# Performance work log

Measured on AMD Instinct MI355X. Metric: run time of the kernel, lower is better.

## Reference

```python
import jax, jax.numpy as jnp
import numpy as np

H = 768
L = 4096
P, KP = 8192, 8
EV, KE = 2048, 6
E = 16384
NR = 32
NUM_LABELS = 2


def setup_inputs() -> dict:
    key = jax.random.key(0)
    ks = jax.random.split(key, 10)
    seq = jax.random.normal(ks[0], (1, L, H), dtype=jnp.float32)
    phrase_idx = jax.random.randint(ks[1], (P, KP), 0, L, dtype=jnp.int32)
    phrase_mask = jnp.ones((P, KP), dtype=jnp.float32)
    event_idx = jax.random.randint(ks[2], (EV, KE), 0, L, dtype=jnp.int32)
    event_mask = jnp.ones((EV, KE), dtype=jnp.float32)
    pair_idx = jax.random.randint(ks[3], (E, 2), 0, EV, dtype=jnp.int32)
    root_idx = jax.random.randint(ks[4], (NR,), 0, P, dtype=jnp.int32)
    s1 = 1.0 / np.sqrt(2 * H)
    W1 = jax.random.normal(ks[5], (2 * H, H), dtype=jnp.float32) * s1
    b1 = jnp.zeros((H,), dtype=jnp.float32)
    Wb = jax.random.normal(ks[6], (2 * H, NUM_LABELS), dtype=jnp.float32) * s1
    bb = jnp.zeros((NUM_LABELS,), dtype=jnp.float32)
    return {"seq": seq, "phrase_idx": phrase_idx, "phrase_mask": phrase_mask,
            "event_idx": event_idx, "event_mask": event_mask, "pair_idx": pair_idx,
            "root_idx": root_idx, "W1": W1, "b1": b1, "Wb": Wb, "bb": bb}


def _masked_mean_gather(tok, idx, mask):
    # tok: [L,H]; idx: [N,K] int; mask: [N,K] float -> [N,H]
    g = tok[idx]                                  # [N,K,H] irregular gather
    s = jnp.einsum('nkh,nk->nh', g, mask)
    d = jnp.maximum(mask.sum(axis=1, keepdims=True), 1.0)
    return s / d


def reference(seq, phrase_idx, phrase_mask, event_idx, event_mask, pair_idx,
              root_idx, W1, b1, Wb, bb):
    tok = seq[0]                                   # [L,H] doc token embeddings
    # phrase embeddings: gather token indices per phrase, masked mean-pool
    ph = _masked_mean_gather(tok, phrase_idx, phrase_mask)   # [P,H]
    # event embeddings: gather span tokens per event, masked mean-pool
    ev = _masked_mean_gather(tok, event_idx, event_mask)     # [EV,H]
    # event-pair nodes: concat the two event embeddings, middle_layer MLP
    e1 = ev[pair_idx[:, 0]]                        # [E,H]
    e2 = ev[pair_idx[:, 1]]                        # [E,H]
    pairs = jnp.concatenate([e1, e2], axis=-1)     # [E,2H]
    node = jax.nn.relu(pairs @ W1 + b1)            # [E,H] (dropout inactive at eval)
    # virtual root: mean of sentence-root phrase embeddings
    vroot = ph[root_idx].mean(axis=0)              # [H]
    feat = jnp.concatenate([node, jnp.broadcast_to(vroot, node.shape)], axis=-1)
    logits = feat @ Wb + bb                        # [E,NUM_LABELS] bilinear classifier
    return logits
```

## Files before the change

kernel.cpp:

```cpp
#include <hip/hip_runtime.h>
#include <hip/hip_bf16.h>

#define H   768
#define H4  192
#define EVN 2048
#define KE  6
#define KP  8
#define EE  16384
#define NR  32

typedef __bf16 v8bf __attribute__((ext_vector_type(8)));
typedef float  v4f  __attribute__((ext_vector_type(4)));

__device__ __forceinline__ void gload16(const void* g, void* lds) {
    __builtin_amdgcn_global_load_lds(
        (const __attribute__((address_space(1))) void*)g,
        (__attribute__((address_space(3))) void*)lds, 16, 0, 0);
}
__device__ __forceinline__ float blo(unsigned u) {
    return __uint_as_float(u << 16);
}
__device__ __forceinline__ float bhi(unsigned u) {
    return __uint_as_float(u & 0xffff0000u);
}

__global__ __launch_bounds__(256) void pre_kernel(
    const float* __restrict__ seq,
    const int* __restrict__ eidx, const float* __restrict__ emask,
    const int* __restrict__ pidx, const float* __restrict__ pmask,
    const int* __restrict__ root_idx, const float* __restrict__ W1,
    __hip_bfloat16* __restrict__ evb, __hip_bfloat16* __restrict__ Wt,
    float* __restrict__ phr) {
    __shared__ float tile[64][65];
    const int b = blockIdx.x;
    const int t = threadIdx.x;
    const float4* seq4 = (const float4*)seq;

    if (b < 512) {
        const int w = t >> 6, l = t & 63;
        const int n = b * 4 + w;
        int idx[KE]; float mk[KE]; float ms = 0.f;
#pragma unroll
        for (int k = 0; k < KE; ++k) {
            idx[k] = eidx[n * KE + k];
            mk[k]  = emask[n * KE + k];
            ms    += mk[k];
        }
        const float inv = 1.f / fmaxf(ms, 1.f);
#pragma unroll
        for (int g = 0; g < 3; ++g) {
            const int t4 = l + g * 64;
            float4 acc = {0.f, 0.f, 0.f, 0.f};
#pragma unroll
            for (int k = 0; k < KE; ++k) {
                float4 v = seq4[idx[k] * H4 + t4];
                acc.x = fmaf(mk[k], v.x, acc.x);
                acc.y = fmaf(mk[k], v.y, acc.y);
                acc.z = fmaf(mk[k], v.z, acc.z);
                acc.w = fmaf(mk[k], v.w, acc.w);
            }
            __hip_bfloat16 o[4];
            o[0] = __float2bfloat16(acc.x * inv);
            o[1] = __float2bfloat16(acc.y * inv);
            o[2] = __float2bfloat16(acc.z * inv);
            o[3] = __float2bfloat16(acc.w * inv);
            *(uint2*)&evb[n * H + t4 * 4] = *(uint2*)o;
        }
    } else if (b < 520) {
        const int w = t >> 6, l = t & 63;
        const int r = (b - 512) * 4 + w;
        const int pr = root_idx[r];
        int idx[KP]; float mk[KP]; float ms = 0.f;
#pragma unroll
        for (int k = 0; k < KP; ++k) {
            idx[k] = pidx[pr * KP + k];
            mk[k]  = pmask[pr * KP + k];
            ms    += mk[k];
        }
        const float inv = 1.f / fmaxf(ms, 1.f);
#pragma unroll
        for (int g = 0; g < 3; ++g) {
            const int t4 = l + g * 64;
            float4 acc = {0.f, 0.f, 0.f, 0.f};
#pragma unroll
            for (int k = 0; k < KP; ++k) {
                float4 v = seq4[idx[k] * H4 + t4];
                acc.x = fmaf(mk[k], v.x, acc.x);
                acc.y = fmaf(mk[k], v.y, acc.y);
                acc.z = fmaf(mk[k], v.z, acc.z);
                acc.w = fmaf(mk[k], v.w, acc.w);
            }
            float4 o = {acc.x * inv, acc.y * inv, acc.z * inv, acc.w * inv};
            ((float4*)phr)[r * H4 + t4] = o;
        }
    } else {
        const int b2 = b - 520;
        const int k0 = (b2 % 12) * 64;
        const int j0 = (b2 / 12) * 64;
        const int s  = (j0 >= H) ? H : 0;
        const int n0 = j0 - s;
        const int c  = t & 63;
        const int r0 = t >> 6;
#pragma unroll
        for (int i = 0; i < 16; ++i) {
            const int r = r0 + i * 4;
            tile[r][c] = W1[(size_t)(s + k0 + r) * H + n0 + c];
        }
        __syncthreads();
#pragma unroll
        for (int i = 0; i < 16; ++i) {
            const int r = r0 + i * 4;
            Wt[(size_t)(j0 + r) * H + k0 + c] = __float2bfloat16(tile[c][r]);
        }
    }
}

__global__ __launch_bounds__(256) void gemm_kernel(
    const __hip_bfloat16* __restrict__ evb_,
    const __hip_bfloat16* __restrict__ Wt_,
    const float* __restrict__ b1v,
    const float* __restrict__ phr, const float* __restrict__ Wb,
    const float* __restrict__ bbv,
    __hip_bfloat16* __restrict__ evw, float* __restrict__ cvec) {
    __shared__ short As[2][16384];

    if (blockIdx.x == 384) {
        float* r0s = (float*)&As[0][0];
        float* r1s = r0s + 256;
        const int t = threadIdx.x;
        float p0 = 0.f, p1 = 0.f;
#pragma unroll
        for (int w = 0; w < 3; ++w) {
            const int d = t + w * 256;
            float s = 0.f;
            for (int r = 0; r < NR; ++r) s += phr[r * H + d];
            const float v = s * (1.0f / NR);
            p0 = fmaf(v, Wb[(H + d) * 2 + 0], p0);
            p1 = fmaf(v, Wb[(H + d) * 2 + 1], p1);
        }
        r0s[t] = p0; r1s[t] = p1;
        __syncthreads();
        for (int off = 128; off > 0; off >>= 1) {
            if (t < off) { r0s[t] += r0s[t + off]; r1s[t] += r1s[t + off]; }
            __syncthreads();
        }
        if (t == 0) { cvec[0] = r0s[0] + bbv[0]; cvec[1] = r1s[0] + bbv[1]; }
        return;
    }

    const short* evb = (const short*)evb_;
    const short* Wt  = (const short*)Wt_;

    const int bid = blockIdx.x;
    const int swz = (bid & 7) * 48 + (bid >> 3);
    const int mt = swz / 24, nt = swz % 24;
    const int m0 = mt * 128, n0 = nt * 64;

    const int t = threadIdx.x;
    const int l = t & 63;
    const int w = t >> 6;
    const int wr = (w >> 1) * 64;
    const int wc = (w & 1) * 32;

    const short* aSrc[8]; int aOff[8];
#pragma unroll
    for (int c = 0; c < 8; ++c) {
        const int s = c * 256 + t;
        const int r = s >> 4, pg = s & 15, g = pg ^ (r & 15);
        aSrc[c] = evb + (size_t)(m0 + r) * H + g * 8;
        aOff[c] = s * 16;
    }

    const int fr = l & 15, gq = l >> 4, xm = fr & 15;
    int aRowB[4];
#pragma unroll
    for (int mi = 0; mi < 4; ++mi) aRowB[mi] = (wr + mi * 16 + fr) * 256;

    const short* bPtr[2];
#pragma unroll
    for (int nj = 0; nj < 2; ++nj)
        bPtr[nj] = Wt + (size_t)(n0 + wc + nj * 16 + fr) * H + gq * 8;

    v4f acc[4][2] = {};
    v8bf bEven[2][4], bOdd[2][4];

#pragma unroll
    for (int nj = 0; nj < 2; ++nj)
#pragma unroll
        for (int h = 0; h < 4; ++h)
            bEven[nj][h] = *(const v8bf*)(bPtr[nj] + h * 32);

#pragma unroll
    for (int c = 0; c < 8; ++c) gload16(aSrc[c], (char*)As[0] + aOff[c]);
    __syncthreads();

#pragma unroll
    for (int ks = 0; ks < 6; ++ks) {
        const int cur = ks & 1;
        if (ks < 5) {
#pragma unroll
            for (int c = 0; c < 8; ++c)
                gload16(aSrc[c] + (ks + 1) * 128, (char*)As[cur ^ 1] + aOff[c]);
#pragma unroll
            for (int nj = 0; nj < 2; ++nj)
#pragma unroll
                for (int h = 0; h < 4; ++h) {
                    v8bf v = *(const v8bf*)(bPtr[nj] + (ks + 1) * 128 + h * 32);
                    if (cur) bEven[nj][h] = v; else bOdd[nj][h] = v;
                }
        }
        const char* Ab = (const char*)As[cur];
#pragma unroll
        for (int h = 0; h < 4; ++h) {
            const int pgo = ((h * 4 + gq) ^ xm) * 16;
            v8bf a0 = *(const v8bf*)(Ab + aRowB[0] + pgo);
            v8bf a1 = *(const v8bf*)(Ab + aRowB[1] + pgo);
            v8bf a2 = *(const v8bf*)(Ab + aRowB[2] + pgo);
            v8bf a3 = *(const v8bf*)(Ab + aRowB[3] + pgo);
            v8bf b0 = cur ? bOdd[0][h] : bEven[0][h];
            v8bf b1 = cur ? bOdd[1][h] : bEven[1][h];
            acc[0][0] = __builtin_amdgcn_mfma_f32_16x16x32_bf16(a0, b0, acc[0][0], 0, 0, 0);
            acc[0][1] = __builtin_amdgcn_mfma_f32_16x16x32_bf16(a0, b1, acc[0][1], 0, 0, 0);
            acc[1][0] = __builtin_amdgcn_mfma_f32_16x16x32_bf16(a1, b0, acc[1][0], 0, 0, 0);
            acc[1][1] = __builtin_amdgcn_mfma_f32_16x16x32_bf16(a1, b1, acc[1][1], 0, 0, 0);
            acc[2][0] = __builtin_amdgcn_mfma_f32_16x16x32_bf16(a2, b0, acc[2][0], 0, 0, 0);
            acc[2][1] = __builtin_amdgcn_mfma_f32_16x16x32_bf16(a2, b1, acc[2][1], 0, 0, 0);
            acc[3][0] = __builtin_amdgcn_mfma_f32_16x16x32_bf16(a3, b0, acc[3][0], 0, 0, 0);
            acc[3][1] = __builtin_amdgcn_mfma_f32_16x16x32_bf16(a3, b1, acc[3][1], 0, 0, 0);
        }
        __syncthreads();
    }

    float bv[2];
#pragma unroll
    for (int nj = 0; nj < 2; ++nj) {
        const int ocol = n0 + wc + nj * 16 + fr;
        bv[nj] = (ocol >= H) ? b1v[ocol - H] : 0.f;
    }
#pragma unroll
    for (int mi = 0; mi < 4; ++mi)
#pragma unroll
        for (int nj = 0; nj < 2; ++nj) {
            const int ocol = n0 + wc + nj * 16 + fr;
#pragma unroll
            for (int r = 0; r < 4; ++r) {
                const int orow = m0 + wr + mi * 16 + gq * 4 + r;
                evw[(size_t)orow * 1536 + ocol] =
                    __float2bfloat16(acc[mi][nj][r] + bv[nj]);
            }
        }
}

__global__ __launch_bounds__(256) void pair_logits_kernel(
    const __hip_bfloat16* __restrict__ evw_, const int* __restrict__ pair_idx,
    const float* __restrict__ Wb, const float* __restrict__ cvec,
    float* __restrict__ out) {
    const ushort* evw = (const ushort*)evw_;
    const int wave = threadIdx.x >> 6;
    const int lane = threadIdx.x & 63;
    const int i = blockIdx.x * 4 + wave;
    const int p0 = pair_idx[i * 2 + 0];
    const int p1 = pair_idx[i * 2 + 1];
    const ushort* ra = evw + (size_t)p0 * 1536;
    const ushort* rb = evw + (size_t)p1 * 1536 + H;
    float acc0 = 0.f, acc1 = 0.f;
#pragma unroll
    for (int h = 0; h < 2; ++h) {
        const int j = h * 384 + lane * 6;
        uint3 ua = *(const uint3*)(ra + j);
        uint3 ub = *(const uint3*)(rb + j);
        float4 w0 = *(const float4*)(Wb + j * 2);
        float4 w1 = *(const float4*)(Wb + j * 2 + 4);
        float4 w2 = *(const float4*)(Wb + j * 2 + 8);
        float n0 = fmaxf(blo(ua.x) + blo(ub.x), 0.f);
        float n1 = fmaxf(bhi(ua.x) + bhi(ub.x), 0.f);
        float n2 = fmaxf(blo(ua.y) + blo(ub.y), 0.f);
        float n3 = fmaxf(bhi(ua.y) + bhi(ub.y), 0.f);
        float n4 = fmaxf(blo(ua.z) + blo(ub.z), 0.f);
        float n5 = fmaxf(bhi(ua.z) + bhi(ub.z), 0.f);
        acc0 += n0 * w0.x + n1 * w0.z + n2 * w1.x + n3 * w1.z + n4 * w2.x + n5 * w2.z;
        acc1 += n0 * w0.y + n1 * w0.w + n2 * w1.y + n3 * w1.w + n4 * w2.y + n5 * w2.w;
    }
#pragma unroll
    for (int off = 32; off > 0; off >>= 1) {
        acc0 += __shfl_xor(acc0, off, 64);
        acc1 += __shfl_xor(acc1, off, 64);
    }
    if (lane == 0) {
        out[i * 2 + 0] = acc0 + cvec[0];
        out[i * 2 + 1] = acc1 + cvec[1];
    }
}

extern "C" void kernel_launch(void* const* d_in, const int* in_sizes, int n_in,
                              void* d_out, int out_size, void* d_ws, size_t ws_size,
                              hipStream_t stream) {
    const float* seq         = (const float*)d_in[0];
    const int*   phrase_idx  = (const int*)  d_in[1];
    const float* phrase_mask = (const float*)d_in[2];
    const int*   event_idx   = (const int*)  d_in[3];
    const float* event_mask  = (const float*)d_in[4];
    const int*   pair_idx    = (const int*)  d_in[5];
    const int*   root_idx    = (const int*)  d_in[6];
    const float* W1          = (const float*)d_in[7];
    const float* b1          = (const float*)d_in[8];
    const float* Wb          = (const float*)d_in[9];
    const float* bb          = (const float*)d_in[10];
    float* out = (float*)d_out;

    char* wsb = (char*)d_ws;
    __hip_bfloat16* evb = (__hip_bfloat16*)wsb;
    __hip_bfloat16* Wt  = (__hip_bfloat16*)(wsb + 3145728);
    __hip_bfloat16* evw = (__hip_bfloat16*)(wsb + 5505024);
    float* phr = (float*)(wsb + 11796480);
    float* c   = (float*)(wsb + 11894784);

    pre_kernel<<<808, 256, 0, stream>>>(seq, event_idx, event_mask,
                                        phrase_idx, phrase_mask, root_idx,
                                        W1, evb, Wt, phr);
    gemm_kernel<<<385, 256, 0, stream>>>(evb, Wt, b1, phr, Wb, bb, evw, c);
    pair_logits_kernel<<<EE / 4, 256, 0, stream>>>(evw, pair_idx, Wb, c, out);
}
```

Measured before the change: 39.16 us.

## Restructure event GEMM into 2-wave, 3-stage LDS pipeline with staged B tiles

The GEMM kernel drops from 4 waves to 2 waves per block, each computing a 64x64 sub-tile with a 4x4 MFMA accumulator grid. K-steps shrink to 64, and both A and the Wt (B) operand are staged through LDS with global_load_lds in a triple-buffered ring. Explicit vmcnt waits replace the per-step __syncthreads, so two tiles stay in flight. The aim is better latency hiding and less register-held B prefetch, at the cost of fewer waves per block and more LDS traffic for B.

After: 33.30 us. -15.0%, faster.

```diff
diff --git a/kernel.cpp b/kernel.cpp
--- a/kernel.cpp
+++ b/kernel.cpp
@@ -115,23 +115,24 @@
     }
 }
 
-__global__ __launch_bounds__(256) void gemm_kernel(
+__global__ __launch_bounds__(128) void gemm_kernel(
     const __hip_bfloat16* __restrict__ evb_,
     const __hip_bfloat16* __restrict__ Wt_,
     const float* __restrict__ b1v,
     const float* __restrict__ phr, const float* __restrict__ Wb,
     const float* __restrict__ bbv,
     __hip_bfloat16* __restrict__ evw, float* __restrict__ cvec) {
-    __shared__ short As[2][16384];
+    __shared__ short As[3][8192];
+    __shared__ short Bs[3][4096];
 
     if (blockIdx.x == 384) {
         float* r0s = (float*)&As[0][0];
-        float* r1s = r0s + 256;
+        float* r1s = r0s + 128;
         const int t = threadIdx.x;
         float p0 = 0.f, p1 = 0.f;
 #pragma unroll
-        for (int w = 0; w < 3; ++w) {
-            const int d = t + w * 256;
+        for (int w = 0; w < 6; ++w) {
+            const int d = t + w * 128;
             float s = 0.f;
             for (int r = 0; r < NR; ++r) s += phr[r * H + d];
             const float v = s * (1.0f / NR);
@@ -140,7 +141,7 @@
         }
         r0s[t] = p0; r1s[t] = p1;
         __syncthreads();
-        for (int off = 128; off > 0; off >>= 1) {
+        for (int off = 64; off > 0; off >>= 1) {
             if (t < off) { r0s[t] += r0s[t + off]; r1s[t] += r1s[t + off]; }
             __syncthreads();
         }
@@ -159,89 +160,96 @@
     const int t = threadIdx.x;
     const int l = t & 63;
     const int w = t >> 6;
-    const int wr = (w >> 1) * 64;
-    const int wc = (w & 1) * 32;
+    const int wr = w * 64;
 
     const short* aSrc[8]; int aOff[8];
 #pragma unroll
     for (int c = 0; c < 8; ++c) {
-        const int s = c * 256 + t;
-        const int r = s >> 4, pg = s & 15, g = pg ^ (r & 15);
+        const int s = c * 128 + t;
+        const int r = s >> 3, pg = s & 7, g = pg ^ (r & 7);
         aSrc[c] = evb + (size_t)(m0 + r) * H + g * 8;
         aOff[c] = s * 16;
     }
-
-    const int fr = l & 15, gq = l >> 4, xm = fr & 15;
-    int aRowB[4];
-#pragma unroll
-    for (int mi = 0; mi < 4; ++mi) aRowB[mi] = (wr + mi * 16 + fr) * 256;
-
-    const short* bPtr[2];
-#pragma unroll
-    for (int nj = 0; nj < 2; ++nj)
-        bPtr[nj] = Wt + (size_t)(n0 + wc + nj * 16 + fr) * H + gq * 8;
-
-    v4f acc[4][2] = {};
-    v8bf bEven[2][4], bOdd[2][4];
-
-#pragma unroll
-    for (int nj = 0; nj < 2; ++nj)
-#pragma unroll
-        for (int h = 0; h < 4; ++h)
-            bEven[nj][h] = *(const v8bf*)(bPtr[nj] + h * 32);
-
-#pragma unroll
-    for (int c = 0; c < 8; ++c) gload16(aSrc[c], (char*)As[0] + aOff[c]);
-    __syncthreads();
-
-#pragma unroll
-    for (int ks = 0; ks < 6; ++ks) {
-        const int cur = ks & 1;
-        if (ks < 5) {
-#pragma unroll
-            for (int c = 0; c < 8; ++c)
-                gload16(aSrc[c] + (ks + 1) * 128, (char*)As[cur ^ 1] + aOff[c]);
-#pragma unroll
-            for (int nj = 0; nj < 2; ++nj)
-#pragma unroll
-                for (int h = 0; h < 4; ++h) {
-                    v8bf v = *(const v8bf*)(bPtr[nj] + (ks + 1) * 128 + h * 32);
-                    if (cur) bEven[nj][h] = v; else bOdd[nj][h] = v;
-                }
-        }
-        const char* Ab = (const char*)As[cur];
-#pragma unroll
-        for (int h = 0; h < 4; ++h) {
-            const int pgo = ((h * 4 + gq) ^ xm) * 16;
+    const short* bSrc[4]; int bOff[4];
+#pragma unroll
+    for (int c = 0; c < 4; ++c) {
+        const int s = c * 128 + t;
+        const int r = s >> 3, pg = s & 7, g = pg ^ (r & 7);
+        bSrc[c] = Wt + (size_t)(n0 + r) * H + g * 8;
+        bOff[c] = s * 16;
+    }
+
+#define STAGE(tile, buf) do {                                              \
+    _Pragma("unroll") for (int c_ = 0; c_ < 8; ++c_)                       \
+        gload16(aSrc[c_] + (tile) * 64, (char*)As[buf] + aOff[c_]);        \
+    _Pragma("unroll") for (int c_ = 0; c_ < 4; ++c_)                       \
+        gload16(bSrc[c_] + (tile) * 64, (char*)Bs[buf] + bOff[c_]);        \
+} while (0)
+
+    const int fr = l & 15, gq = l >> 4, xm = fr & 7;
+    int aRowB[4], bRowB[4];
+#pragma unroll
+    for (int mi = 0; mi < 4; ++mi) aRowB[mi] = (wr + mi * 16 + fr) * 128;
+#pragma unroll
+    for (int nj = 0; nj < 4; ++nj) bRowB[nj] = (nj * 16 + fr) * 128;
+
+    v4f acc[4][4] = {};
+
+    STAGE(0, 0);
+    STAGE(1, 1);
+
+#pragma unroll
+    for (int ks = 0; ks < 12; ++ks) {
+        if (ks < 11) { asm volatile("s_waitcnt vmcnt(12)" ::: "memory"); }
+        else         { asm volatile("s_waitcnt vmcnt(0)"  ::: "memory"); }
+        __builtin_amdgcn_sched_barrier(0);
+        __builtin_amdgcn_s_barrier();
+        __builtin_amdgcn_sched_barrier(0);
+        if (ks < 10) STAGE(ks + 2, (ks + 2) % 3);
+        const char* Ab = (const char*)As[ks % 3];
+        const char* Bb = (const char*)Bs[ks % 3];
+#pragma unroll
+        for (int hh = 0; hh < 2; ++hh) {
+            const int pgo = ((hh * 4 + gq) ^ xm) * 16;
             v8bf a0 = *(const v8bf*)(Ab + aRowB[0] + pgo);
             v8bf a1 = *(const v8bf*)(Ab + aRowB[1] + pgo);
             v8bf a2 = *(const v8bf*)(Ab + aRowB[2] + pgo);
             v8bf a3 = *(const v8bf*)(Ab + aRowB[3] + pgo);
-            v8bf b0 = cur ? bOdd[0][h] : bEven[0][h];
-            v8bf b1 = cur ? bOdd[1][h] : bEven[1][h];
+            v8bf b0 = *(const v8bf*)(Bb + bRowB[0] + pgo);
+            v8bf b1 = *(const v8bf*)(Bb + bRowB[1] + pgo);
+            v8bf b2 = *(const v8bf*)(Bb + bRowB[2] + pgo);
+            v8bf b3 = *(const v8bf*)(Bb + bRowB[3] + pgo);
             acc[0][0] = __builtin_amdgcn_mfma_f32_16x16x32_bf16(a0, b0, acc[0][0], 0, 0, 0);
             acc[0][1] = __builtin_amdgcn_mfma_f32_16x16x32_bf16(a0, b1, acc[0][1], 0, 0, 0);
+            acc[0][2] = __builtin_amdgcn_mfma_f32_16x16x32_bf16(a0, b2, acc[0][2], 0, 0, 0);
+            acc[0][3] = __builtin_amdgcn_mfma_f32_16x16x32_bf16(a0, b3, acc[0][3], 0, 0, 0);
             acc[1][0] = __builtin_amdgcn_mfma_f32_16x16x32_bf16(a1, b0, acc[1][0], 0, 0, 0);
             acc[1][1] = __builtin_amdgcn_mfma_f32_16x16x32_bf16(a1, b1, acc[1][1], 0, 0, 0);
+            acc[1][2] = __builtin_amdgcn_mfma_f32_16x16x32_bf16(a1, b2, acc[1][2], 0, 0, 0);
+            acc[1][3] = __builtin_amdgcn_mfma_f32_16x16x32_bf16(a1, b3, acc[1][3], 0, 0, 0);
             acc[2][0] = __builtin_amdgcn_mfma_f32_16x16x32_bf16(a2, b0, acc[2][0], 0, 0, 0);
             acc[2][1] = __builtin_amdgcn_mfma_f32_16x16x32_bf16(a2, b1, acc[2][1], 0, 0, 0);
+            acc[2][2] = __builtin_amdgcn_mfma_f32_16x16x32_bf16(a2, b2, acc[2][2], 0, 0, 0);
+            acc[2][3] = __builtin_amdgcn_mfma_f32_16x16x32_bf16(a2, b3, acc[2][3], 0, 0, 0);
             acc[3][0] = __builtin_amdgcn_mfma_f32_16x16x32_bf16(a3, b0, acc[3][0], 0, 0, 0);
             acc[3][1] = __builtin_amdgcn_mfma_f32_16x16x32_bf16(a3, b1, acc[3][1], 0, 0, 0);
-        }
-        __syncthreads();
-    }
-
-    float bv[2];
-#pragma unroll
-    for (int nj = 0; nj < 2; ++nj) {
-        const int ocol = n0 + wc + nj * 16 + fr;
+            acc[3][2] = __builtin_amdgcn_mfma_f32_16x16x32_bf16(a3, b2, acc[3][2], 0, 0, 0);
+            acc[3][3] = __builtin_amdgcn_mfma_f32_16x16x32_bf16(a3, b3, acc[3][3], 0, 0, 0);
+        }
+    }
+#undef STAGE
+
+    float bv[4];
+#pragma unroll
+    for (int nj = 0; nj < 4; ++nj) {
+        const int ocol = n0 + nj * 16 + fr;
         bv[nj] = (ocol >= H) ? b1v[ocol - H] : 0.f;
     }
 #pragma unroll
     for (int mi = 0; mi < 4; ++mi)
 #pragma unroll
-        for (int nj = 0; nj < 2; ++nj) {
-            const int ocol = n0 + wc + nj * 16 + fr;
+        for (int nj = 0; nj < 4; ++nj) {
+            const int ocol = n0 + nj * 16 + fr;
 #pragma unroll
             for (int r = 0; r < 4; ++r) {
                 const int orow = m0 + wr + mi * 16 + gq * 4 + r;
@@ -318,6 +326,6 @@
     pre_kernel<<<808, 256, 0, stream>>>(seq, event_idx, event_mask,
                                         phrase_idx, phrase_mask, root_idx,
                                         W1, evb, Wt, phr);
-    gemm_kernel<<<385, 256, 0, stream>>>(evb, Wt, b1, phr, Wb, bb, evw, c);
+    gemm_kernel<<<385, 128, 0, stream>>>(evb, Wt, b1, phr, Wb, bb, evw, c);
     pair_logits_kernel<<<EE / 4, 256, 0, stream>>>(evw, pair_idx, Wb, c, out);
 }
```
